# Kernel optimization log

Measured on AMD Instinct MI355X. Metric: run time of the kernel, lower is better.

## Reference

```python
import jax, jax.numpy as jnp
import numpy as np

L, D = 8192, 1024


def binary_operator_diag(q_i, q_j):
    # elementwise (diagonal) linear-recurrence combine: h_j = A_j * h_i + b_j
    A_i, b_i = q_i
    A_j, b_j = q_j
    return A_j * A_i, A_j * b_i + b_j


def setup_inputs() -> dict:
    key = jax.random.key(0)
    k_in, k_u, k_th, k_bre, k_bim = jax.random.split(key, 5)
    inputs = jax.random.normal(k_in, (L, D), dtype=jnp.float32)
    # stable LRU init: |lambda| = exp(-exp(nu)) = sqrt(u), u in (0.01, 0.99)
    u = jax.random.uniform(k_u, (D,), jnp.float32, 0.01, 0.99)
    nu = jnp.log(-0.5 * jnp.log(u))
    # phase stored in log-space (forward uses exp(theta))
    theta = jnp.log(jax.random.uniform(k_th, (D,), jnp.float32, 1e-3, 6.28))
    gamma_log = 0.5 * jnp.log(1.0 - u)  # = log(sqrt(1 - |lambda|^2))
    norm = np.float32(np.sqrt(2.0 * D))
    B_re = jax.random.normal(k_bre, (D, D), jnp.float32) / norm
    B_im = jax.random.normal(k_bim, (D, D), jnp.float32) / norm
    return {"inputs": inputs, "theta": theta, "nu": nu,
            "gamma_log": gamma_log, "B_re": B_re, "B_im": B_im}


def reference(inputs, theta, nu, gamma_log, B_re, B_im):
    # diagonal transition: lambda = exp(-exp(nu) + i*exp(theta)), shape [D]
    diag_lambda = jnp.exp(-jnp.exp(nu) + 1j * jnp.exp(theta))
    # normalized input matrix: (B_re + i B_im) * exp(gamma_log)[:, None]
    B_norm = (B_re + 1j * B_im) * jnp.exp(gamma_log)[:, None]  # [D, D] complex
    # Bu[t] = B_norm @ u_t  -> batched as one GEMM: [L, D] complex
    Bu = jnp.einsum('ld,kd->lk', inputs.astype(B_norm.dtype), B_norm)
    Lambda_elements = jnp.broadcast_to(diag_lambda[None, :], Bu.shape)
    # parallel associative scan over time (axis 0), elementwise over channels
    _, hidden_states = jax.lax.associative_scan(
        binary_operator_diag, (Lambda_elements, Bu))
    return hidden_states.real + inputs
```

## Files before the change

### kernel.cpp

```cpp
#include <hip/hip_runtime.h>
#include <cstdint>
#include <cstddef>

typedef float  f32x4   __attribute__((ext_vector_type(4)));
typedef float  f32x16  __attribute__((ext_vector_type(16)));
typedef short  bf16x8  __attribute__((ext_vector_type(8)));
typedef unsigned short u16x8 __attribute__((ext_vector_type(8)));

#define L_SEQ   8192
#define D_DIM   1024
#define N_COL   2048
#define N_PAIR  512
#define CHUNK_T 16
#define N_CHUNK 512

__device__ __forceinline__ unsigned short f2bf(float f) {
  unsigned int b = __float_as_uint(f);
  b += 0x7FFFu + ((b >> 16) & 1u);
  return (unsigned short)(b >> 16);
}
__device__ __forceinline__ float bf2f(unsigned short u) {
  return __uint_as_float((unsigned int)u << 16);
}
__device__ __forceinline__ void gload_lds16(const void* g, void* lds) {
  __builtin_amdgcn_global_load_lds(
      (const __attribute__((address_space(1))) void*)g,
      (__attribute__((address_space(3))) void*)lds, 16, 0, 0);
}
__device__ __forceinline__ float2 cmul(float2 a, float2 b) {
  return make_float2(a.x * b.x - a.y * b.y, a.x * b.y + a.y * b.x);
}
__device__ __forceinline__ float2 csqr(float2 a) {
  return make_float2(a.x * a.x - a.y * a.y, 2.f * a.x * a.y);
}
__device__ __forceinline__ void cfma2(const float4& lm, float2& h0, float2& h1,
                                      const float4& v) {
  float nr0 = fmaf(lm.x, h0.x, fmaf(-lm.y, h0.y, v.x));
  float ni0 = fmaf(lm.x, h0.y, fmaf(lm.y, h0.x, v.y));
  float nr1 = fmaf(lm.z, h1.x, fmaf(-lm.w, h1.y, v.z));
  float ni1 = fmaf(lm.z, h1.y, fmaf(lm.w, h1.x, v.w));
  h0.x = nr0; h0.y = ni0; h1.x = nr1; h1.y = ni1;
}

__global__ __launch_bounds__(256) void k_prep(
    const float* __restrict__ in, const float* __restrict__ Bre,
    const float* __restrict__ Bim, const float* __restrict__ gamma_log,
    const float* __restrict__ theta, const float* __restrict__ nu,
    unsigned short* __restrict__ A, unsigned short* __restrict__ W,
    float2* __restrict__ lam) {
  int b = blockIdx.x;
  if (b < 4096) {
    int i = b * 256 + threadIdx.x;
    const float4* p = (const float4*)in;
    float4 a = p[2 * i], c = p[2 * i + 1];
    u16x8 o;
    o[0] = f2bf(a.x); o[1] = f2bf(a.y); o[2] = f2bf(a.z); o[3] = f2bf(a.w);
    o[4] = f2bf(c.x); o[5] = f2bf(c.y); o[6] = f2bf(c.z); o[7] = f2bf(c.w);
    *(u16x8*)(A + (size_t)i * 8) = o;
  } else if (b < 5120) {
    int t = (b - 4096) * 256 + threadIdx.x;
    int row = t >> 7;
    int seg = t & 127;
    int k = row >> 1;
    const float* src = (row & 1) ? Bim : Bre;
    float g = expf(gamma_log[k]);
    const float4* p = (const float4*)(src + (size_t)k * D_DIM + seg * 8);
    float4 a = p[0], c = p[1];
    u16x8 o;
    o[0] = f2bf(a.x * g); o[1] = f2bf(a.y * g); o[2] = f2bf(a.z * g); o[3] = f2bf(a.w * g);
    o[4] = f2bf(c.x * g); o[5] = f2bf(c.y * g); o[6] = f2bf(c.z * g); o[7] = f2bf(c.w * g);
    *(u16x8*)(W + (size_t)row * D_DIM + seg * 8) = o;
  } else {
    int k = (b - 5120) * 256 + threadIdx.x;
    if (k < D_DIM) {
      float mod = expf(-expf(nu[k]));
      float ang = expf(theta[k]);
      lam[k] = make_float2(mod * cosf(ang), mod * sinf(ang));
    }
  }
}

__global__ __launch_bounds__(512, 1) void k_gemm(const unsigned short* __restrict__ A,
                                                 const unsigned short* __restrict__ W,
                                                 unsigned short* __restrict__ Bu16,
                                                 float2* __restrict__ agg2,
                                                 const float2* __restrict__ lam) {
  extern __shared__ char smem[];

  const int tid = threadIdx.x;
  const int l = tid & 63, w = tid >> 6;
  const int wm = w >> 2, wn = w & 3;

  int orig = blockIdx.x;
  int wgid = (orig & 7) * 32 + (orig >> 3);
  const int mt = wgid >> 3, nt = wgid & 7;
  const size_t m0 = (size_t)mt * 256, n0 = (size_t)nt * 256;

  const size_t srcoff0 = (size_t)(tid & 127) * 2048 + (size_t)(tid >> 7) * 16;
  const size_t srcoff1 = srcoff0 + 64;
  const int dst0 = tid * 16, dst1 = 8192 + tid * 16;

#define STAGE(Mptr, Mbase, Msel, bb, hh, TT) do {                                   \
    const char* s_ = (const char*)(Mptr) +                                          \
        (((Mbase) + (size_t)(hh) * 128) * 2048 + (size_t)(TT) * 128);               \
    char* d_ = smem + (Msel) * 65536 + (bb) * 32768 + (hh) * 16384;                 \
    gload_lds16(s_ + srcoff0, d_ + dst0);                                           \
    gload_lds16(s_ + srcoff1, d_ + dst1);                                           \
  } while (0)

  int aroff[4], broff[2];
#pragma unroll
  for (int mb = 0; mb < 4; ++mb) {
    int lrow = wm * 128 + mb * 32 + (l & 31);
    aroff[mb] = (lrow >> 7) * 16384 + (lrow & 127) * 16;
  }
#pragma unroll
  for (int nb = 0; nb < 2; ++nb) {
    int lrow = wn * 64 + nb * 32 + (l & 31);
    broff[nb] = (lrow >> 7) * 16384 + (lrow & 127) * 16;
  }
  int swk[4];
#pragma unroll
  for (int ks = 0; ks < 4; ++ks)
    swk[ks] = (ks * 2 + (l >> 5)) * 2048;

  f32x16 acc[4][2];
#pragma unroll
  for (int mb = 0; mb < 4; ++mb)
#pragma unroll
    for (int nb = 0; nb < 2; ++nb)
#pragma unroll
      for (int r = 0; r < 16; ++r) acc[mb][nb][r] = 0.f;

  bf16x8 af[2][4], bfr[2][4];

#define LGKMC0 asm volatile("s_waitcnt lgkmcnt(0)" ::: "memory")
#define VMCNT4 asm volatile("s_waitcnt vmcnt(4)" ::: "memory")
#define VMCNT0 asm volatile("s_waitcnt vmcnt(0)" ::: "memory")
#define BAR()  do { asm volatile("" ::: "memory"); __builtin_amdgcn_s_barrier(); \
                    asm volatile("" ::: "memory"); } while (0)

  STAGE(W, n0, 1, 0, 0, 0);
  STAGE(A, m0, 0, 0, 1, 0);
  STAGE(A, m0, 0, 0, 0, 0);
  STAGE(W, n0, 1, 0, 1, 0);
  STAGE(W, n0, 1, 1, 0, 1);
  STAGE(A, m0, 0, 1, 1, 1);
  VMCNT4;
  BAR();

  for (int kt = 0; kt < 16; ++kt) {
    const int buf = kt & 1;
    const int abase = buf * 32768;
    const int bbase = 65536 + buf * 32768;
    const int b1 = (kt + 1) & 1, b2 = kt & 1;
    const bool s1 = (kt + 1 < 16), s2 = (kt + 2 < 16);

#pragma unroll
    for (int mb = 0; mb < 2; ++mb)
#pragma unroll
      for (int ks = 0; ks < 4; ++ks)
        af[mb][ks] = *(const bf16x8*)(smem + abase + aroff[mb] + swk[ks]);
#pragma unroll
    for (int ks = 0; ks < 4; ++ks)
      bfr[0][ks] = *(const bf16x8*)(smem + bbase + broff[0] + swk[ks]);
    if (s1) STAGE(A, m0, 0, b1, 0, kt + 1);
    __builtin_amdgcn_s_setprio(1);
#pragma unroll
    for (int mb = 0; mb < 2; ++mb)
#pragma unroll
      for (int ks = 0; ks < 4; ++ks)
        acc[mb][0] = __builtin_amdgcn_mfma_f32_32x32x16_bf16(af[mb][ks], bfr[0][ks],
                                                             acc[mb][0], 0, 0, 0);
    __builtin_amdgcn_s_setprio(0);
    LGKMC0;
    BAR();

#pragma unroll
    for (int ks = 0; ks < 4; ++ks)
      bfr[1][ks] = *(const bf16x8*)(smem + bbase + broff[1] + swk[ks]);
    if (s1) STAGE(W, n0, 1, b1, 1, kt + 1);
    __builtin_amdgcn_s_setprio(1);
#pragma unroll
    for (int mb = 0; mb < 2; ++mb)
#pragma unroll
      for (int ks = 0; ks < 4; ++ks)
        acc[mb][1] = __builtin_amdgcn_mfma_f32_32x32x16_bf16(af[mb][ks], bfr[1][ks],
                                                             acc[mb][1], 0, 0, 0);
    __builtin_amdgcn_s_setprio(0);
    LGKMC0;
    BAR();

#pragma unroll
    for (int mb = 0; mb < 2; ++mb)
#pragma unroll
      for (int ks = 0; ks < 4; ++ks)
        af[mb][ks] = *(const bf16x8*)(smem + abase + aroff[2 + mb] + swk[ks]);
    if (s2) STAGE(W, n0, 1, b2, 0, kt + 2);
    __builtin_amdgcn_s_setprio(1);
#pragma unroll
    for (int mb = 0; mb < 2; ++mb)
#pragma unroll
      for (int ks = 0; ks < 4; ++ks)
        acc[2 + mb][1] = __builtin_amdgcn_mfma_f32_32x32x16_bf16(af[mb][ks], bfr[1][ks],
                                                                 acc[2 + mb][1], 0, 0, 0);
    __builtin_amdgcn_s_setprio(0);
    LGKMC0;
    BAR();

    if (s2) STAGE(A, m0, 0, b2, 1, kt + 2);
    __builtin_amdgcn_s_setprio(1);
#pragma unroll
    for (int mb = 0; mb < 2; ++mb)
#pragma unroll
      for (int ks = 0; ks < 4; ++ks)
        acc[2 + mb][0] = __builtin_amdgcn_mfma_f32_32x32x16_bf16(af[mb][ks], bfr[0][ks],
                                                                 acc[2 + mb][0], 0, 0, 0);
    __builtin_amdgcn_s_setprio(0);
    if (kt < 14) VMCNT4; else VMCNT0;
    BAR();
  }
#undef STAGE

#pragma unroll
  for (int mb = 0; mb < 4; ++mb)
#pragma unroll
    for (int nb = 0; nb < 2; ++nb) {
      int col = wn * 64 + nb * 32 + (l & 31);
#pragma unroll
      for (int r = 0; r < 16; ++r) {
        int row = wm * 128 + mb * 32 + (r & 3) + 8 * (r >> 2) + 4 * (l >> 5);
        int byte = row * 512 + ((col * 2) ^ ((row & 7) << 4));
        *(unsigned short*)(smem + byte) = f2bf(acc[mb][nb][r]);
      }
    }
  __syncthreads();

  {
    unsigned short* gbase = Bu16 + m0 * N_COL + n0;
#pragma unroll
    for (int pass = 0; pass < 16; ++pass) {
      int row = pass * 16 + (tid >> 5);
      int c = tid & 31;
      int byte = row * 512 + ((c * 16) ^ ((row & 7) << 4));
      f32x4 v = *(const f32x4*)(smem + byte);
      *(f32x4*)(gbase + (size_t)row * N_COL + c * 8) = v;
    }
  }

#pragma unroll
  for (int i = 0; i < 4; ++i) {
    int q = i * 512 + tid;
    int c = q >> 7, ch = q & 127;
    float2 lmv = lam[(n0 >> 1) + ch];
    unsigned int pr[16];
#pragma unroll
    for (int s = 0; s < 16; ++s) {
      int row = c * 16 + s;
      pr[s] = *(const unsigned int*)(smem + row * 512 + ((ch * 4) ^ ((row & 7) << 4)));
    }
    float2 h = {0.f, 0.f};
#pragma unroll
    for (int s = 0; s < 16; ++s) {
      float br = bf2f((unsigned short)(pr[s] & 0xFFFFu));
      float bi = bf2f((unsigned short)(pr[s] >> 16));
      float nr = fmaf(lmv.x, h.x, fmaf(-lmv.y, h.y, br));
      float ni = fmaf(lmv.x, h.y, fmaf(lmv.y, h.x, bi));
      h.x = nr; h.y = ni;
    }
    agg2[(size_t)(mt * 16 + c) * 1024 + (n0 >> 1) + ch] = h;
  }
}

__global__ __launch_bounds__(256) void k_scan2(const float4* __restrict__ agg4,
                                               const float4* __restrict__ lam4,
                                               float4* __restrict__ carry4) {
  int wave = blockIdx.x * 4 + (threadIdx.x >> 6);
  int lane = threadIdx.x & 63;
  int j = wave;
  float4 lm = lam4[j];
  float2 lT0 = {lm.x, lm.y}, lT1 = {lm.z, lm.w};
#pragma unroll
  for (int i = 0; i < 4; ++i) { lT0 = csqr(lT0); lT1 = csqr(lT1); }

  float4 a[8];
  float2 T0 = {0.f, 0.f}, T1 = {0.f, 0.f};
  float4 lTv = make_float4(lT0.x, lT0.y, lT1.x, lT1.y);
#pragma unroll
  for (int i = 0; i < 8; ++i) {
    a[i] = agg4[(size_t)(lane * 8 + i) * N_PAIR + j];
    cfma2(lTv, T0, T1, a[i]);
  }

  float2 M0 = lT0, M1 = lT1;
#pragma unroll
  for (int i = 0; i < 3; ++i) { M0 = csqr(M0); M1 = csqr(M1); }
  float2 S0 = T0, S1 = T1;
#pragma unroll
  for (int d = 1; d < 64; d <<= 1) {
    float2 u0, u1;
    u0.x = __shfl_up(S0.x, d); u0.y = __shfl_up(S0.y, d);
    u1.x = __shfl_up(S1.x, d); u1.y = __shfl_up(S1.y, d);
    if (lane >= d) {
      float2 m0 = cmul(M0, u0), m1 = cmul(M1, u1);
      S0.x += m0.x; S0.y += m0.y; S1.x += m1.x; S1.y += m1.y;
    }
    M0 = csqr(M0); M1 = csqr(M1);
  }
  float2 P0, P1;
  P0.x = __shfl_up(S0.x, 1); P0.y = __shfl_up(S0.y, 1);
  P1.x = __shfl_up(S1.x, 1); P1.y = __shfl_up(S1.y, 1);
  if (lane == 0) { P0 = make_float2(0.f, 0.f); P1 = make_float2(0.f, 0.f); }

#pragma unroll
  for (int i = 0; i < 8; ++i) {
    carry4[(size_t)(lane * 8 + i) * N_PAIR + j] = make_float4(P0.x, P0.y, P1.x, P1.y);
    cfma2(lTv, P0, P1, a[i]);
  }
}

__global__ __launch_bounds__(256) void k_scan3(const u16x8* __restrict__ Bu8,
                                               const float4* __restrict__ lam4,
                                               const float4* __restrict__ carry4,
                                               const ushort4* __restrict__ inA,
                                               float4* __restrict__ out4) {
  int t = blockIdx.x * 256 + threadIdx.x;
  int c = t >> 8, q = t & 255;
  float4 lm0 = lam4[2 * q], lm1 = lam4[2 * q + 1];
  float4 cv0 = carry4[(size_t)c * N_PAIR + 2 * q];
  float4 cv1 = carry4[(size_t)c * N_PAIR + 2 * q + 1];
  float2 h0 = {cv0.x, cv0.y}, h1 = {cv0.z, cv0.w};
  float2 h2 = {cv1.x, cv1.y}, h3 = {cv1.z, cv1.w};
#pragma unroll
  for (int s = 0; s < CHUNK_T; ++s) {
    size_t row = (size_t)c * CHUNK_T + s;
    u16x8 b = Bu8[row * 256 + q];
    float4 v0 = make_float4(bf2f(b[0]), bf2f(b[1]), bf2f(b[2]), bf2f(b[3]));
    float4 v1 = make_float4(bf2f(b[4]), bf2f(b[5]), bf2f(b[6]), bf2f(b[7]));
    cfma2(lm0, h0, h1, v0);
    cfma2(lm1, h2, h3, v1);
    ushort4 iv = inA[row * 256 + q];
    out4[row * 256 + q] = make_float4(h0.x + bf2f(iv.x), h1.x + bf2f(iv.y),
                                      h2.x + bf2f(iv.z), h3.x + bf2f(iv.w));
  }
}

extern "C" void kernel_launch(void* const* d_in, const int* in_sizes, int n_in,
                              void* d_out, int out_size, void* d_ws, size_t ws_size,
                              hipStream_t stream) {
  (void)in_sizes; (void)n_in; (void)out_size; (void)ws_size;
  const float* inputs    = (const float*)d_in[0];
  const float* theta     = (const float*)d_in[1];
  const float* nu        = (const float*)d_in[2];
  const float* gamma_log = (const float*)d_in[3];
  const float* Bre       = (const float*)d_in[4];
  const float* Bim       = (const float*)d_in[5];

  char* ws = (char*)d_ws;
  float2*         lam   = (float2*)ws;
  unsigned short* A     = (unsigned short*)(ws + (1 << 16));
  unsigned short* W     = (unsigned short*)(ws + (1 << 16) + (16u << 20));
  unsigned short* Bu16  = (unsigned short*)(ws + (1 << 16) + (20u << 20));
  float2*         agg   = (float2*)(ws + (1 << 16) + (52u << 20));
  float4*         carry = (float4*)(ws + (1 << 16) + (56u << 20));

  hipFuncSetAttribute((const void*)k_gemm,
                      hipFuncAttributeMaxDynamicSharedMemorySize, 131072);

  k_prep<<<5124, 256, 0, stream>>>(inputs, Bre, Bim, gamma_log, theta, nu, A, W, lam);
  k_gemm<<<256, 512, 131072, stream>>>(A, W, Bu16, agg, (const float2*)lam);
  k_scan2<<<N_PAIR / 4, 256, 0, stream>>>((const float4*)agg, (const float4*)lam, carry);
  k_scan3<<<(N_CHUNK * 256) / 256, 256, 0, stream>>>((const u16x8*)Bu16,
                                                     (const float4*)lam, carry,
                                                     (const ushort4*)A,
                                                     (float4*)d_out);
}
```

Baseline: 78.13 us.

## Shrink GEMM tile to 256x128 with 3-stage pipeline and 16x16 MFMA

```diff
diff --git a/kernel.cpp b/kernel.cpp
--- a/kernel.cpp
+++ b/kernel.cpp
@@ -3,7 +3,6 @@
 #include <cstddef>
 
 typedef float  f32x4   __attribute__((ext_vector_type(4)));
-typedef float  f32x16  __attribute__((ext_vector_type(16)));
 typedef short  bf16x8  __attribute__((ext_vector_type(8)));
 typedef unsigned short u16x8 __attribute__((ext_vector_type(8)));
 
@@ -80,7 +79,7 @@
   }
 }
 
-__global__ __launch_bounds__(512, 1) void k_gemm(const unsigned short* __restrict__ A,
+__global__ __launch_bounds__(512, 4) void k_gemm(const unsigned short* __restrict__ A,
                                                  const unsigned short* __restrict__ W,
                                                  unsigned short* __restrict__ Bu16,
                                                  float2* __restrict__ agg2,
@@ -89,149 +88,88 @@
 
   const int tid = threadIdx.x;
   const int l = tid & 63, w = tid >> 6;
-  const int wm = w >> 2, wn = w & 3;
+  const int wm = w >> 1, wn = w & 1;
 
   int orig = blockIdx.x;
-  int wgid = (orig & 7) * 32 + (orig >> 3);
-  const int mt = wgid >> 3, nt = wgid & 7;
-  const size_t m0 = (size_t)mt * 256, n0 = (size_t)nt * 256;
-
-  const size_t srcoff0 = (size_t)(tid & 127) * 2048 + (size_t)(tid >> 7) * 16;
-  const size_t srcoff1 = srcoff0 + 64;
-  const int dst0 = tid * 16, dst1 = 8192 + tid * 16;
-
-#define STAGE(Mptr, Mbase, Msel, bb, hh, TT) do {                                   \
-    const char* s_ = (const char*)(Mptr) +                                          \
-        (((Mbase) + (size_t)(hh) * 128) * 2048 + (size_t)(TT) * 128);               \
-    char* d_ = smem + (Msel) * 65536 + (bb) * 32768 + (hh) * 16384;                 \
-    gload_lds16(s_ + srcoff0, d_ + dst0);                                           \
-    gload_lds16(s_ + srcoff1, d_ + dst1);                                           \
+  int wgid = (orig & 7) * 64 + (orig >> 3);
+  const int mt = wgid >> 4, nt = wgid & 15;
+  const size_t m0 = (size_t)mt * 256, n0 = (size_t)nt * 128;
+
+#define STAGE_A(bb, TT) do {                                                        \
+    const char* s_ = (const char*)A + m0 * 2048 + (size_t)(TT) * 64;                \
+    char* d_ = smem + (bb) * 16384;                                                 \
+    gload_lds16(s_ + (size_t)(tid >> 2) * 2048 + (tid & 3) * 16, d_ + tid * 16);    \
+    gload_lds16(s_ + (size_t)(128 + (tid >> 2)) * 2048 + (tid & 3) * 16,            \
+                d_ + 8192 + tid * 16);                                              \
   } while (0)
-
-  int aroff[4], broff[2];
-#pragma unroll
-  for (int mb = 0; mb < 4; ++mb) {
-    int lrow = wm * 128 + mb * 32 + (l & 31);
-    aroff[mb] = (lrow >> 7) * 16384 + (lrow & 127) * 16;
-  }
-#pragma unroll
-  for (int nb = 0; nb < 2; ++nb) {
-    int lrow = wn * 64 + nb * 32 + (l & 31);
-    broff[nb] = (lrow >> 7) * 16384 + (lrow & 127) * 16;
-  }
-  int swk[4];
-#pragma unroll
-  for (int ks = 0; ks < 4; ++ks)
-    swk[ks] = (ks * 2 + (l >> 5)) * 2048;
-
-  f32x16 acc[4][2];
-#pragma unroll
-  for (int mb = 0; mb < 4; ++mb)
-#pragma unroll
-    for (int nb = 0; nb < 2; ++nb)
-#pragma unroll
-      for (int r = 0; r < 16; ++r) acc[mb][nb][r] = 0.f;
-
-  bf16x8 af[2][4], bfr[2][4];
-
-#define LGKMC0 asm volatile("s_waitcnt lgkmcnt(0)" ::: "memory")
-#define VMCNT4 asm volatile("s_waitcnt vmcnt(4)" ::: "memory")
+#define STAGE_B(bb, TT) do {                                                        \
+    const char* s_ = (const char*)W + n0 * 2048 + (size_t)(TT) * 64;                \
+    char* d_ = smem + 49152 + (bb) * 8192;                                          \
+    gload_lds16(s_ + (size_t)(tid >> 2) * 2048 + (tid & 3) * 16, d_ + tid * 16);    \
+  } while (0)
+
+  int aoff[4], boff[4];
+#pragma unroll
+  for (int fr = 0; fr < 4; ++fr)
+    aoff[fr] = (wm * 64 + fr * 16 + (l & 15)) * 64 + (l >> 4) * 16;
+#pragma unroll
+  for (int fn = 0; fn < 4; ++fn)
+    boff[fn] = (wn * 64 + fn * 16 + (l & 15)) * 64 + (l >> 4) * 16;
+
+  f32x4 acc[4][4];
+#pragma unroll
+  for (int m = 0; m < 4; ++m)
+#pragma unroll
+    for (int n = 0; n < 4; ++n) acc[m][n] = (f32x4){0.f, 0.f, 0.f, 0.f};
+
+#define VMCNT3 asm volatile("s_waitcnt vmcnt(3)" ::: "memory")
 #define VMCNT0 asm volatile("s_waitcnt vmcnt(0)" ::: "memory")
 #define BAR()  do { asm volatile("" ::: "memory"); __builtin_amdgcn_s_barrier(); \
                     asm volatile("" ::: "memory"); } while (0)
 
-  STAGE(W, n0, 1, 0, 0, 0);
-  STAGE(A, m0, 0, 0, 1, 0);
-  STAGE(A, m0, 0, 0, 0, 0);
-  STAGE(W, n0, 1, 0, 1, 0);
-  STAGE(W, n0, 1, 1, 0, 1);
-  STAGE(A, m0, 0, 1, 1, 1);
-  VMCNT4;
+  STAGE_A(0, 0); STAGE_B(0, 0);
+  STAGE_A(1, 1); STAGE_B(1, 1);
+  VMCNT3;
   BAR();
 
-  for (int kt = 0; kt < 16; ++kt) {
-    const int buf = kt & 1;
-    const int abase = buf * 32768;
-    const int bbase = 65536 + buf * 32768;
-    const int b1 = (kt + 1) & 1, b2 = kt & 1;
-    const bool s1 = (kt + 1 < 16), s2 = (kt + 2 < 16);
-
-#pragma unroll
-    for (int mb = 0; mb < 2; ++mb)
-#pragma unroll
-      for (int ks = 0; ks < 4; ++ks)
-        af[mb][ks] = *(const bf16x8*)(smem + abase + aroff[mb] + swk[ks]);
-#pragma unroll
-    for (int ks = 0; ks < 4; ++ks)
-      bfr[0][ks] = *(const bf16x8*)(smem + bbase + broff[0] + swk[ks]);
-    if (s1) STAGE(A, m0, 0, b1, 0, kt + 1);
+  for (int kt = 0; kt < 32; ++kt) {
+    const int rb = kt % 3;
+    if (kt + 2 < 32) {
+      const int nb = (kt + 2) % 3;
+      STAGE_A(nb, kt + 2);
+      STAGE_B(nb, kt + 2);
+    }
+    const char* ab = smem + rb * 16384;
+    const char* bb = smem + 49152 + rb * 8192;
+    bf16x8 a_[4], b_[4];
+#pragma unroll
+    for (int fr = 0; fr < 4; ++fr) a_[fr] = *(const bf16x8*)(ab + aoff[fr]);
+#pragma unroll
+    for (int fn = 0; fn < 4; ++fn) b_[fn] = *(const bf16x8*)(bb + boff[fn]);
     __builtin_amdgcn_s_setprio(1);
 #pragma unroll
-    for (int mb = 0; mb < 2; ++mb)
-#pragma unroll
-      for (int ks = 0; ks < 4; ++ks)
-        acc[mb][0] = __builtin_amdgcn_mfma_f32_32x32x16_bf16(af[mb][ks], bfr[0][ks],
-                                                             acc[mb][0], 0, 0, 0);
+    for (int fr = 0; fr < 4; ++fr)
+#pragma unroll
+      for (int fn = 0; fn < 4; ++fn)
+        acc[fr][fn] = __builtin_amdgcn_mfma_f32_16x16x32_bf16(a_[fr], b_[fn],
+                                                              acc[fr][fn], 0, 0, 0);
     __builtin_amdgcn_s_setprio(0);
-    LGKMC0;
+    if (kt < 30) VMCNT3; else VMCNT0;
     BAR();
-
-#pragma unroll
-    for (int ks = 0; ks < 4; ++ks)
-      bfr[1][ks] = *(const bf16x8*)(smem + bbase + broff[1] + swk[ks]);
-    if (s1) STAGE(W, n0, 1, b1, 1, kt + 1);
-    __builtin_amdgcn_s_setprio(1);
-#pragma unroll
-    for (int mb = 0; mb < 2; ++mb)
-#pragma unroll
-      for (int ks = 0; ks < 4; ++ks)
-        acc[mb][1] = __builtin_amdgcn_mfma_f32_32x32x16_bf16(af[mb][ks], bfr[1][ks],
-                                                             acc[mb][1], 0, 0, 0);
-    __builtin_amdgcn_s_setprio(0);
-    LGKMC0;
-    BAR();
-
-#pragma unroll
-    for (int mb = 0; mb < 2; ++mb)
-#pragma unroll
-      for (int ks = 0; ks < 4; ++ks)
-        af[mb][ks] = *(const bf16x8*)(smem + abase + aroff[2 + mb] + swk[ks]);
-    if (s2) STAGE(W, n0, 1, b2, 0, kt + 2);
-    __builtin_amdgcn_s_setprio(1);
-#pragma unroll
-    for (int mb = 0; mb < 2; ++mb)
-#pragma unroll
-      for (int ks = 0; ks < 4; ++ks)
-        acc[2 + mb][1] = __builtin_amdgcn_mfma_f32_32x32x16_bf16(af[mb][ks], bfr[1][ks],
-                                                                 acc[2 + mb][1], 0, 0, 0);
-    __builtin_amdgcn_s_setprio(0);
-    LGKMC0;
-    BAR();
-
-    if (s2) STAGE(A, m0, 0, b2, 1, kt + 2);
-    __builtin_amdgcn_s_setprio(1);
-#pragma unroll
-    for (int mb = 0; mb < 2; ++mb)
-#pragma unroll
-      for (int ks = 0; ks < 4; ++ks)
-        acc[2 + mb][0] = __builtin_amdgcn_mfma_f32_32x32x16_bf16(af[mb][ks], bfr[0][ks],
-                                                                 acc[2 + mb][0], 0, 0, 0);
-    __builtin_amdgcn_s_setprio(0);
-    if (kt < 14) VMCNT4; else VMCNT0;
-    BAR();
-  }
-#undef STAGE
-
-#pragma unroll
-  for (int mb = 0; mb < 4; ++mb)
-#pragma unroll
-    for (int nb = 0; nb < 2; ++nb) {
-      int col = wn * 64 + nb * 32 + (l & 31);
-#pragma unroll
-      for (int r = 0; r < 16; ++r) {
-        int row = wm * 128 + mb * 32 + (r & 3) + 8 * (r >> 2) + 4 * (l >> 5);
-        int byte = row * 512 + ((col * 2) ^ ((row & 7) << 4));
-        *(unsigned short*)(smem + byte) = f2bf(acc[mb][nb][r]);
+  }
+#undef STAGE_A
+#undef STAGE_B
+
+#pragma unroll
+  for (int fr = 0; fr < 4; ++fr)
+#pragma unroll
+    for (int fn = 0; fn < 4; ++fn) {
+      int col = wn * 64 + fn * 16 + (l & 15);
+#pragma unroll
+      for (int j = 0; j < 4; ++j) {
+        int row = wm * 64 + fr * 16 + (l >> 4) * 4 + j;
+        int byte = row * 256 + ((col * 2) ^ ((row & 7) << 4));
+        *(unsigned short*)(smem + byte) = f2bf(acc[fr][fn][j]);
       }
     }
   __syncthreads();
@@ -239,25 +177,25 @@
   {
     unsigned short* gbase = Bu16 + m0 * N_COL + n0;
 #pragma unroll
-    for (int pass = 0; pass < 16; ++pass) {
-      int row = pass * 16 + (tid >> 5);
-      int c = tid & 31;
-      int byte = row * 512 + ((c * 16) ^ ((row & 7) << 4));
+    for (int pass = 0; pass < 8; ++pass) {
+      int row = pass * 32 + (tid >> 4);
+      int c = tid & 15;
+      int byte = row * 256 + ((c * 16) ^ ((row & 7) << 4));
       f32x4 v = *(const f32x4*)(smem + byte);
       *(f32x4*)(gbase + (size_t)row * N_COL + c * 8) = v;
     }
   }
 
 #pragma unroll
-  for (int i = 0; i < 4; ++i) {
+  for (int i = 0; i < 2; ++i) {
     int q = i * 512 + tid;
-    int c = q >> 7, ch = q & 127;
+    int c = q >> 6, ch = q & 63;
     float2 lmv = lam[(n0 >> 1) + ch];
     unsigned int pr[16];
 #pragma unroll
     for (int s = 0; s < 16; ++s) {
       int row = c * 16 + s;
-      pr[s] = *(const unsigned int*)(smem + row * 512 + ((ch * 4) ^ ((row & 7) << 4)));
+      pr[s] = *(const unsigned int*)(smem + row * 256 + ((ch * 4) ^ ((row & 7) << 4)));
     }
     float2 h = {0.f, 0.f};
 #pragma unroll
@@ -365,10 +303,10 @@
   float4*         carry = (float4*)(ws + (1 << 16) + (56u << 20));
 
   hipFuncSetAttribute((const void*)k_gemm,
-                      hipFuncAttributeMaxDynamicSharedMemorySize, 131072);
+                      hipFuncAttributeMaxDynamicSharedMemorySize, 73728);
 
   k_prep<<<5124, 256, 0, stream>>>(inputs, Bre, Bim, gamma_log, theta, nu, A, W, lam);
-  k_gemm<<<256, 512, 131072, stream>>>(A, W, Bu16, agg, (const float2*)lam);
+  k_gemm<<<512, 512, 73728, stream>>>(A, W, Bu16, agg, (const float2*)lam);
   k_scan2<<<N_PAIR / 4, 256, 0, stream>>>((const float4*)agg, (const float4*)lam, carry);
   k_scan3<<<(N_CHUNK * 256) / 256, 256, 0, stream>>>((const u16x8*)Bu16,
                                                      (const float4*)lam, carry,
```

Result: faster. 74.58 us (-4.5%).
